# Performance work log

Hardware: AMD Instinct MI355X
Metric: run time of the kernel (lower is better)

The kernel has to match this reference:

```python
import jax, jax.numpy as jnp
import numpy as np

B, T, D, H, BUCKETS = 4, 4096, 1024, 8, 64
DH = D // H          # 128
BSZ = T // BUCKETS   # 64
TEMP = 0.75
SINK_ITERS = 5
LOG_EPS = 1e-6
GUMBEL_EPS = 1e-4


def setup_inputs() -> dict:
    key = jax.random.key(0)
    ks = jax.random.split(key, 6)
    x = jax.random.normal(ks[0], (B, T, D), dtype=jnp.float32)
    w_qkv = jax.random.normal(ks[1], (3 * D, D), dtype=jnp.float32) * 0.02   # torch Linear weight (out,in), no bias
    sort_w = jax.random.normal(ks[2], (1, H, DH, BUCKETS), dtype=jnp.float32)
    w_out = jax.random.normal(ks[3], (D, D), dtype=jnp.float32) * 0.02
    b_out = jnp.zeros((D,), dtype=jnp.float32)
    noise_u = jax.random.uniform(ks[4], (B * H, BUCKETS, BUCKETS), dtype=jnp.float32)
    return {"x": x, "w_qkv": w_qkv, "sort_w": sort_w, "w_out": w_out, "b_out": b_out, "noise_u": noise_u}


def reference(x, w_qkv, sort_w, w_out, b_out, noise_u):
    b, t, d = x.shape
    # qkv projection + merge heads -> (b*h, t, d_h)
    qkv = x @ w_qkv.T
    q, k, v = jnp.split(qkv, 3, axis=2)
    mh = lambda u: u.reshape(b, t, H, DH).transpose(0, 2, 1, 3).reshape(b * H, t, DH)
    q, k, v = mh(q), mh(k), mh(v)
    # bucket -> (b*h, buckets, bsz, d_h)
    bk = lambda u: u.reshape(b * H, BUCKETS, BSZ, DH)
    b_q, b_k, b_v = bk(q), bk(k), bk(v)
    # bucket summaries and sinkhorn sorting matrix R: (b*h, buckets, buckets)
    b_k_r = b_k.sum(axis=2)
    e_w = jnp.broadcast_to(sort_w, (b, H, DH, BUCKETS)).reshape(b * H, DH, BUCKETS)
    R = jnp.log(jax.nn.relu(jnp.einsum('bud,bdv->buv', b_k_r, e_w)) + LOG_EPS)
    gumbel = -jnp.log(-jnp.log(noise_u + GUMBEL_EPS) + GUMBEL_EPS)
    R = (R + gumbel) / TEMP
    for _ in range(SINK_ITERS):
        R = R - jax.nn.logsumexp(R, axis=2, keepdims=True)
        R = R - jax.nn.logsumexp(R, axis=1, keepdims=True)
    R = jnp.tril(jnp.exp(R), k=-1)
    # soft-permute buckets of k and v
    k_re = jnp.einsum('buv,bvtd->butd', R, b_k)
    v_re = jnp.einsum('buv,bvtd->butd', R, b_v)
    b_k2 = jnp.concatenate((k_re, b_k), axis=2)  # (bh, buckets, 2*bsz, dh)
    b_v2 = jnp.concatenate((v_re, b_v), axis=2)
    # bucketed attention (note: scale uses full model dim d, as in source)
    dots = jnp.einsum('buie,buje->buij', b_q, b_k2) * (d ** -0.5)
    attn = jax.nn.softmax(dots, axis=-1)
    out = jnp.einsum('buij,buje->buie', attn, b_v2)
    # unbucket + split heads -> (b, t, d)
    out = out.reshape(b, H, t, DH).transpose(0, 2, 1, 3).reshape(b, t, d)
    return out @ w_out.T + b_out
```

## Files before the change

### kernel.cpp

```cpp
#include <hip/hip_runtime.h>
#include <hip/hip_bf16.h>
#include <cstdint>
#include <cstddef>
#include <math.h>
#include <type_traits>

typedef __bf16 bf16;
typedef __bf16 bf16x4 __attribute__((ext_vector_type(4)));
typedef __bf16 bf16x8 __attribute__((ext_vector_type(8)));
typedef float  f32x4  __attribute__((ext_vector_type(4)));
typedef unsigned u32x2 __attribute__((ext_vector_type(2)));


__device__ inline bool input_is_fp32(const void* x) {
  const unsigned short* u = (const unsigned short*)x;
  const int lane = threadIdx.x & 63;
  const int e = (u[lane] >> 7) & 0xFF;
  return __ballot(e >= 137) != 0ULL;
}

__device__ inline float ldx(const void* p, size_t i, bool f32) {
  return f32 ? ((const float*)p)[i] : (float)((const bf16*)p)[i];
}

template<typename T>
__device__ inline bf16x8 ld8bf(const void* p, size_t i) {
  if constexpr (std::is_same<T, float>::value) {
    const f32x4* q = (const f32x4*)((const float*)p + i);
    const f32x4 a = q[0], b = q[1];
    bf16x8 r;
    r[0]=(bf16)a[0]; r[1]=(bf16)a[1]; r[2]=(bf16)a[2]; r[3]=(bf16)a[3];
    r[4]=(bf16)b[0]; r[5]=(bf16)b[1]; r[6]=(bf16)b[2]; r[7]=(bf16)b[3];
    return r;
  } else {
    return *(const bf16x8*)((const bf16*)p + i);
  }
}

__device__ __forceinline__ void gload16(const void* g, void* l) {
  __builtin_amdgcn_global_load_lds(
      (__attribute__((address_space(1))) void*)g,
      (__attribute__((address_space(3))) void*)l, 16, 0, 0);
}

__global__ __launch_bounds__(256)
void convert_to_bf16(const void* __restrict__ src, bf16* __restrict__ dst,
                     const void* __restrict__ xdet) {
  const bool f32 = input_is_fp32(xdet);
  const size_t i = ((size_t)blockIdx.x * 256 + threadIdx.x) * 8;
  if (f32) *(bf16x8*)&dst[i] = ld8bf<float>(src, i);
  else     *(bf16x8*)&dst[i] = ld8bf<bf16 >(src, i);
}

template<int EPI>
__global__ __launch_bounds__(256)
void gemm_bt(const bf16* __restrict__ A, const bf16* __restrict__ Bm,
             const void* __restrict__ bias,
             void* __restrict__ C0, bf16* __restrict__ C1, bf16* __restrict__ C2,
             const void* __restrict__ xdet, int M, int N, int K)
{
  __shared__ __align__(16) bf16 As[128*32];
  __shared__ __align__(16) bf16 Bs[128*32];
  const int tid  = threadIdx.x;
  const int wave = tid >> 6, lane = tid & 63;
  const int m0 = blockIdx.y * 128, n0 = blockIdx.x * 128;
  const int wm = (wave >> 1) * 64, wn = (wave & 1) * 64;
  const int fr = lane & 15;
  const int fk = (lane >> 4) * 8;

  const int srow = wave * 16 + (lane >> 2);
  const int scol = (lane & 3) * 8;
  const bf16* gA = A  + (size_t)(m0 + srow) * K + scol;
  const bf16* gB = Bm + (size_t)(n0 + srow) * K + scol;
  bf16* lA = &As[wave * 16 * 32];
  bf16* lB = &Bs[wave * 16 * 32];

  f32x4 acc[4][4];
  #pragma unroll
  for (int a = 0; a < 4; ++a)
    #pragma unroll
    for (int b = 0; b < 4; ++b) { f32x4 z = {0.f, 0.f, 0.f, 0.f}; acc[a][b] = z; }

  for (int k0 = 0; k0 < K; k0 += 32) {
    __syncthreads();
    gload16(gA + k0,                  lA);
    gload16(gA + (size_t)64*K + k0,   lA + 64*32);
    gload16(gB + k0,                  lB);
    gload16(gB + (size_t)64*K + k0,   lB + 64*32);
    __syncthreads();
    bf16x8 af[4], bfr[4];
    #pragma unroll
    for (int t = 0; t < 4; ++t) {
      af[t]  = *(const bf16x8*)&As[(wm + t*16 + fr)*32 + fk];
      bfr[t] = *(const bf16x8*)&Bs[(wn + t*16 + fr)*32 + fk];
    }
    #pragma unroll
    for (int tm = 0; tm < 4; ++tm)
      #pragma unroll
      for (int tn = 0; tn < 4; ++tn)
        acc[tm][tn] = __builtin_amdgcn_mfma_f32_16x16x32_bf16(af[tm], bfr[tn], acc[tm][tn], 0, 0, 0);
  }

  const int cn = lane & 15, cr = (lane >> 4) * 4;
  if constexpr (EPI == 0) {
    const int sel = n0 >> 10;
    const int cb  = (n0 & 1023) + wn;
    #pragma unroll
    for (int tm = 0; tm < 4; ++tm) {
      const int m = m0 + wm + tm*16 + cr;
      const int b = m >> 12, t = m & 4095;
      const int u = t >> 6,  i = t & 63;
      #pragma unroll
      for (int tn = 0; tn < 4; ++tn) {
        const int c = cb + tn*16 + cn;
        const int h = c >> 7, e = c & 127;
        const size_t bhu = (size_t)((b*8 + h)*64 + u);
        if (sel == 2) {
          bf16x4 w;
          #pragma unroll
          for (int r = 0; r < 4; ++r) w[r] = (bf16)acc[tm][tn][r];
          *(bf16x4*)&C2[(bhu*128 + e)*64 + i] = w;
        } else {
          bf16* dst = (sel == 0) ? (bf16*)C0 : C1;
          #pragma unroll
          for (int r = 0; r < 4; ++r)
            dst[(bhu*64 + i + r)*128 + e] = (bf16)acc[tm][tn][r];
        }
      }
    }
  } else {
    const bool f32o = input_is_fp32(xdet);
    #pragma unroll
    for (int tm = 0; tm < 4; ++tm) {
      #pragma unroll
      for (int tn = 0; tn < 4; ++tn) {
        #pragma unroll
        for (int r = 0; r < 4; ++r) {
          const int m = m0 + wm + tm*16 + cr + r;
          const int n = n0 + wn + tn*16 + cn;
          const float val = acc[tm][tn][r] + ldx(bias, n, f32o);
          if (f32o) ((float*)C0)[(size_t)m*N + n] = val;
          else      ((bf16*)C0)[(size_t)m*N + n] = (bf16)val;
        }
      }
    }
  }
}

__global__ __launch_bounds__(128)
void bksum(const bf16* __restrict__ k_ws, float* __restrict__ bkr_g)
{
  const int ug = blockIdx.x, bh = blockIdx.y, t = threadIdx.x;
  const int ul = t >> 4, e0 = (t & 15) * 8;
  const int u = ug * 8 + ul;
  const bf16* p = k_ws + ((size_t)bh*64 + u)*8192 + e0;
  float acc[8];
  #pragma unroll
  for (int j = 0; j < 8; ++j) acc[j] = 0.f;
  for (int i = 0; i < 64; ++i) {
    bf16x8 kv = *(const bf16x8*)&p[i*128];
    #pragma unroll
    for (int j = 0; j < 8; ++j) acc[j] += (float)kv[j];
  }
  float* dst = bkr_g + (size_t)bh*8192 + u*128 + e0;
  #pragma unroll
  for (int j = 0; j < 8; ++j) dst[j] = acc[j];
}

__global__ __launch_bounds__(256)
void sinkhorn_R(const float* __restrict__ bkr_g, const void* __restrict__ sort_w,
                const void* __restrict__ noise, float* __restrict__ R_buf,
                const void* __restrict__ xdet)
{
  const bool f32 = input_is_fp32(xdet);
  const int bh = blockIdx.x, h = bh & 7, tid = threadIdx.x;
  __shared__ float bkr[64*128];
  __shared__ float ew[128*64];
  __shared__ float R[64*65];

  for (int f = tid; f < 64*128; f += 256) bkr[f] = bkr_g[(size_t)bh*8192 + f];
  for (int f = tid; f < 128*64; f += 256) ew[f] = ldx(sort_w, (size_t)h*8192 + f, f32);
  __syncthreads();

  for (int f = tid; f < 64*64; f += 256) {
    const int u = f >> 6, v = f & 63;
    float s = 0.f;
    for (int e = 0; e < 128; ++e) s += bkr[u*128 + e] * ew[e*64 + v];
    s = fmaxf(s, 0.f);
    const float r  = logf(s + 1e-6f);
    const double nz = (double)ldx(noise, ((size_t)bh*64 + u)*64 + v, f32);
    const double t1 = log(nz + 1e-4);
    const double t2 = fmax(-t1 + 1e-4, 1e-30);
    const float g = (float)(-log(t2));
    R[u*65 + v] = (r + g) * (1.f / 0.75f);
  }
  __syncthreads();

  for (int it = 0; it < 5; ++it) {
    if (tid < 64) {
      float mx = -1e30f;
      for (int v = 0; v < 64; ++v) mx = fmaxf(mx, R[tid*65 + v]);
      float s = 0.f;
      for (int v = 0; v < 64; ++v) s += expf(R[tid*65 + v] - mx);
      const float l = mx + logf(s);
      for (int v = 0; v < 64; ++v) R[tid*65 + v] -= l;
    }
    __syncthreads();
    if (tid < 64) {
      float mx = -1e30f;
      for (int u = 0; u < 64; ++u) mx = fmaxf(mx, R[u*65 + tid]);
      float s = 0.f;
      for (int u = 0; u < 64; ++u) s += expf(R[u*65 + tid] - mx);
      const float l = mx + logf(s);
      for (int u = 0; u < 64; ++u) R[u*65 + tid] -= l;
    }
    __syncthreads();
  }

  for (int f = tid; f < 64*64; f += 256) {
    const int u = f >> 6, v = f & 63;
    R_buf[(size_t)bh*4096 + f] = (u > v) ? expf(R[u*65 + v]) : 0.f;
  }
}

__global__ __launch_bounds__(256)
void permute_kv(const float* __restrict__ R_buf,
                const bf16* __restrict__ Xk, const bf16* __restrict__ Xv,
                bf16* __restrict__ Ok, bf16* __restrict__ Ov, int bh0)
{
  const int tid = threadIdx.x;
  const int bhl = blockIdx.y, bh = bh0 + bhl;
  const int f0  = blockIdx.x * 256;
  const bf16* X = blockIdx.z ? Xv : Xk;
  bf16*       O = blockIdx.z ? Ov : Ok;

  __shared__ __align__(16) bf16 A_lds[64*136];
  __shared__ __align__(16) bf16 X_lds[16*1048];

  {
    const bf16* Xg = X + (size_t)bh*524288 + f0;
    const int vb = tid >> 5, c = tid & 31;
    const int dst = (c >> 1)*1048 + (c & 1)*8;
    #pragma unroll
    for (int p = 0; p < 8; ++p) {
      const int v = vb + p*8;
      *(bf16x8*)&X_lds[dst + v*16] = *(const bf16x8*)&Xg[(size_t)v*8192 + c*8];
    }
  }
  {
    const float* Rg = R_buf + (size_t)bh*4096;
    #pragma unroll
    for (int p = 0; p < 16; ++p) {
      const int idx = tid + p*256;
      const int uu = idx >> 6, vv = idx & 63;
      const float r = Rg[idx];
      const bf16 hi = (bf16)r;
      const float lo = r - (float)hi;
      A_lds[uu*136 + vv]      = hi;
      A_lds[uu*136 + 64 + vv] = (bf16)lo;
    }
  }
  __syncthreads();

  const int lane = tid & 63, wave = tid >> 6;
  const int fr = lane & 15, quad = lane >> 4;

  bf16x8 af[4][4];
  #pragma unroll
  for (int mt = 0; mt < 4; ++mt)
    #pragma unroll
    for (int ks = 0; ks < 4; ++ks)
      af[mt][ks] = *(const bf16x8*)&A_lds[(mt*16 + fr)*136 + ks*32 + quad*8];

  f32x4 acc[4][4];
  #pragma unroll
  for (int a = 0; a < 4; ++a)
    #pragma unroll
    for (int b = 0; b < 4; ++b) { f32x4 z = {0.f,0.f,0.f,0.f}; acc[a][b] = z; }

  #pragma unroll
  for (int nt = 0; nt < 4; ++nt) {
    const int g = wave*4 + nt;
    const unsigned addr = (unsigned)(size_t)
        (__attribute__((address_space(3))) bf16*)&X_lds[g*1048 + quad*128 + fr*4];
    u32x2 p0, p1, p2, p3;
    asm volatile(
      "ds_read_b64_tr_b16 %0, %4\n"
      "ds_read_b64_tr_b16 %1, %4 offset:128\n"
      "ds_read_b64_tr_b16 %2, %4 offset:1024\n"
      "ds_read_b64_tr_b16 %3, %4 offset:1152\n"
      : "=&v"(p0), "=&v"(p1), "=&v"(p2), "=&v"(p3)
      : "v"(addr));
    asm volatile("s_waitcnt lgkmcnt(0)" ::: "memory");
    __builtin_amdgcn_sched_barrier(0);
    union { u32x2 u[2]; bf16x8 v; } c0, c1;
    c0.u[0] = p0; c0.u[1] = p1;
    c1.u[0] = p2; c1.u[1] = p3;
    const bf16x8 b0 = c0.v, b1 = c1.v;
    #pragma unroll
    for (int mt = 0; mt < 4; ++mt) {
      acc[mt][nt] = __builtin_amdgcn_mfma_f32_16x16x32_bf16(af[mt][0], b0, acc[mt][nt], 0, 0, 0);
      acc[mt][nt] = __builtin_amdgcn_mfma_f32_16x16x32_bf16(af[mt][1], b1, acc[mt][nt], 0, 0, 0);
      acc[mt][nt] = __builtin_amdgcn_mfma_f32_16x16x32_bf16(af[mt][2], b0, acc[mt][nt], 0, 0, 0);
      acc[mt][nt] = __builtin_amdgcn_mfma_f32_16x16x32_bf16(af[mt][3], b1, acc[mt][nt], 0, 0, 0);
    }
  }

  bf16* Og = O + (size_t)bhl*524288 + f0;
  #pragma unroll
  for (int mt = 0; mt < 4; ++mt)
    #pragma unroll
    for (int nt = 0; nt < 4; ++nt)
      #pragma unroll
      for (int r = 0; r < 4; ++r)
        Og[(size_t)(mt*16 + quad*4 + r)*8192 + wave*64 + nt*16 + fr] = (bf16)acc[mt][nt][r];
}

__global__ __launch_bounds__(256)
void attn_mfma(const bf16* __restrict__ q_ws, const bf16* __restrict__ k_ws,
               const bf16* __restrict__ vT_ws,
               const bf16* __restrict__ kre_g, const bf16* __restrict__ vre_g,
               bf16* __restrict__ aout, int bh0)
{
  const int u = blockIdx.x, bhl = blockIdx.y, bh = bh0 + bhl;
  const int tid = threadIdx.x;
  const int lane = tid & 63, wave = tid >> 6;
  const int fr = lane & 15, quad = lane >> 4;

  __shared__ __align__(16) unsigned char smem[34048];
  float* sc = (float*)smem;
  bf16*  pA = (bf16*)smem;

  const size_t tileq = ((size_t)bh *64 + u) * 8192;
  const size_t tilel = ((size_t)bhl*64 + u) * 8192;

  {
    f32x4 dacc[4][2];
    #pragma unroll
    for (int mt = 0; mt < 4; ++mt)
      #pragma unroll
      for (int nt = 0; nt < 2; ++nt) { f32x4 z = {0.f,0.f,0.f,0.f}; dacc[mt][nt] = z; }
    #pragma unroll
    for (int ks = 0; ks < 4; ++ks) {
      bf16x8 afr[4];
      #pragma unroll
      for (int mt = 0; mt < 4; ++mt)
        afr[mt] = *(const bf16x8*)&q_ws[tileq + (size_t)(mt*16 + fr)*128 + ks*32 + quad*8];
      #pragma unroll
      for (int nt = 0; nt < 2; ++nt) {
        const int j = wave*32 + nt*16 + fr;
        bf16x8 bfr;
        if (wave < 2) bfr = *(const bf16x8*)&kre_g[tilel + (size_t)j*128 + ks*32 + quad*8];
        else          bfr = *(const bf16x8*)&k_ws[tileq + (size_t)(j - 64)*128 + ks*32 + quad*8];
        #pragma unroll
        for (int mt = 0; mt < 4; ++mt)
          dacc[mt][nt] = __builtin_amdgcn_mfma_f32_16x16x32_bf16(afr[mt], bfr, dacc[mt][nt], 0, 0, 0);
      }
    }
    #pragma unroll
    for (int mt = 0; mt < 4; ++mt)
      #pragma unroll
      for (int nt = 0; nt < 2; ++nt)
        #pragma unroll
        for (int r = 0; r < 4; ++r)
          sc[(mt*16 + quad*4 + r)*132 + wave*32 + nt*16 + fr] = dacc[mt][nt][r] * 0.03125f;
  }
  __syncthreads();

  {
    const int i = tid >> 2, jc = tid & 3;
    float pv[32];
    float mx = -1e30f;
    #pragma unroll
    for (int t = 0; t < 32; ++t) { pv[t] = sc[i*132 + jc + t*4]; mx = fmaxf(mx, pv[t]); }
    mx = fmaxf(mx, __shfl_xor(mx, 1));
    mx = fmaxf(mx, __shfl_xor(mx, 2));
    float s = 0.f;
    #pragma unroll
    for (int t = 0; t < 32; ++t) { pv[t] = expf(pv[t] - mx); s += pv[t]; }
    s += __shfl_xor(s, 1);
    s += __shfl_xor(s, 2);
    const float inv = 1.f / s;
    __syncthreads();
    #pragma unroll
    for (int t = 0; t < 32; ++t) pA[i*136 + jc + t*4] = (bf16)(pv[t] * inv);
  }
  __syncthreads();

  {
    f32x4 oacc[4][2];
    #pragma unroll
    for (int mt = 0; mt < 4; ++mt)
      #pragma unroll
      for (int nt = 0; nt < 2; ++nt) { f32x4 z = {0.f,0.f,0.f,0.f}; oacc[mt][nt] = z; }
    #pragma unroll
    for (int ks = 0; ks < 4; ++ks) {
      bf16x8 afr[4];
      #pragma unroll
      for (int mt = 0; mt < 4; ++mt)
        afr[mt] = *(const bf16x8*)&pA[(mt*16 + fr)*136 + ks*32 + quad*8];
      #pragma unroll
      for (int nt = 0; nt < 2; ++nt) {
        const int e = wave*32 + nt*16 + fr;
        bf16x8 bfr;
        if (ks < 2) bfr = *(const bf16x8*)&vre_g[tilel + (size_t)e*64 + ks*32 + quad*8];
        else        bfr = *(const bf16x8*)&vT_ws[tileq + (size_t)e*64 + (ks - 2)*32 + quad*8];
        #pragma unroll
        for (int mt = 0; mt < 4; ++mt)
          oacc[mt][nt] = __builtin_amdgcn_mfma_f32_16x16x32_bf16(afr[mt], bfr, oacc[mt][nt], 0, 0, 0);
      }
    }
    __syncthreads();
    #pragma unroll
    for (int mt = 0; mt < 4; ++mt)
      #pragma unroll
      for (int nt = 0; nt < 2; ++nt)
        #pragma unroll
        for (int r = 0; r < 4; ++r)
          pA[(mt*16 + quad*4 + r)*136 + wave*32 + nt*16 + fr] = (bf16)oacc[mt][nt][r];
  }
  __syncthreads();

  {
    const int b = bh >> 3, h = bh & 7;
    #pragma unroll
    for (int r = 0; r < 4; ++r) {
      const int f = r*2048 + tid*8;
      const int i = f >> 7, e0 = f & 127;
      bf16x8 w = *(const bf16x8*)&pA[i*136 + e0];
      *(bf16x8*)&aout[((size_t)(b*4096 + u*64 + i))*1024 + h*128 + e0] = w;
    }
  }
}

extern "C" void kernel_launch(void* const* d_in, const int* in_sizes, int n_in,
                              void* d_out, int out_size, void* d_ws, size_t ws_size,
                              hipStream_t stream)
{
  (void)in_sizes; (void)n_in; (void)out_size; (void)ws_size;
  const void* x      = d_in[0];
  const void* w_qkv  = d_in[1];
  const void* sort_w = d_in[2];
  const void* w_out  = d_in[3];
  const void* b_out  = d_in[4];
  const void* noise  = d_in[5];

  char* ws = (char*)d_ws;
  const size_t TEN = (size_t)32*64*64*128;
  const size_t HEN = TEN / 2;
  bf16* q_ws  = (bf16*)ws;
  bf16* k_ws  = q_ws + TEN;
  bf16* vT_ws = k_ws + TEN;
  bf16* xa_ws = vT_ws + TEN;

  float* bkr_g = (float*)((char*)xa_ws + (size_t)30*1024*1024);
  float* R_buf = (float*)((char*)xa_ws + (size_t)31*1024*1024);
  bf16* wqkv_bf = (bf16*)((char*)d_out + (1536<<10));
  bf16* kre = (bf16*)d_out;
  bf16* vre = kre + HEN;
  bf16* wout_bf = k_ws;

  convert_to_bf16<<<8192, 256, 0, stream>>>(x, xa_ws, x);
  convert_to_bf16<<<1536, 256, 0, stream>>>(w_qkv, wqkv_bf, x);

  gemm_bt<0><<<dim3(24,128), 256, 0, stream>>>(xa_ws, wqkv_bf, nullptr,
                                               q_ws, k_ws, vT_ws, x, 16384, 3072, 1024);

  bksum<<<dim3(8,32), 128, 0, stream>>>(k_ws, bkr_g);
  sinkhorn_R<<<32, 256, 0, stream>>>(bkr_g, sort_w, noise, R_buf, x);

  permute_kv<<<dim3(32,16,2), 256, 0, stream>>>(R_buf, k_ws, vT_ws, kre, vre, 0);
  attn_mfma<<<dim3(64,16), 256, 0, stream>>>(q_ws, k_ws, vT_ws, kre, vre, xa_ws, 0);
  permute_kv<<<dim3(32,16,2), 256, 0, stream>>>(R_buf, k_ws, vT_ws, kre, vre, 16);
  attn_mfma<<<dim3(64,16), 256, 0, stream>>>(q_ws, k_ws, vT_ws, kre, vre, xa_ws, 16);

  convert_to_bf16<<<512, 256, 0, stream>>>(w_out, wout_bf, x);
  gemm_bt<1><<<dim3(8,128), 256, 0, stream>>>(xa_ws, wout_bf, b_out,
                                              d_out, nullptr, nullptr, x, 16384, 1024, 1024);
}
```

Before: 479.2 us.

## Replace GEMM with 256x256 tile double-buffered pipelined kernel with swizzled LDS

```diff
diff --git a/kernel.cpp b/kernel.cpp
--- a/kernel.cpp
+++ b/kernel.cpp
@@ -53,92 +53,166 @@
 }
 
 template<int EPI>
-__global__ __launch_bounds__(256)
-void gemm_bt(const bf16* __restrict__ A, const bf16* __restrict__ Bm,
+__global__ __launch_bounds__(512, 2)
+void gemm256(const bf16* __restrict__ A, const bf16* __restrict__ Bm,
              const void* __restrict__ bias,
              void* __restrict__ C0, bf16* __restrict__ C1, bf16* __restrict__ C2,
              const void* __restrict__ xdet, int M, int N, int K)
 {
-  __shared__ __align__(16) bf16 As[128*32];
-  __shared__ __align__(16) bf16 Bs[128*32];
-  const int tid  = threadIdx.x;
-  const int wave = tid >> 6, lane = tid & 63;
-  const int m0 = blockIdx.y * 128, n0 = blockIdx.x * 128;
-  const int wm = (wave >> 1) * 64, wn = (wave & 1) * 64;
-  const int fr = lane & 15;
-  const int fk = (lane >> 4) * 8;
-
-  const int srow = wave * 16 + (lane >> 2);
-  const int scol = (lane & 3) * 8;
-  const bf16* gA = A  + (size_t)(m0 + srow) * K + scol;
-  const bf16* gB = Bm + (size_t)(n0 + srow) * K + scol;
-  bf16* lA = &As[wave * 16 * 32];
-  bf16* lB = &Bs[wave * 16 * 32];
-
-  f32x4 acc[4][4];
-  #pragma unroll
-  for (int a = 0; a < 4; ++a)
-    #pragma unroll
-    for (int b = 0; b < 4; ++b) { f32x4 z = {0.f, 0.f, 0.f, 0.f}; acc[a][b] = z; }
-
-  for (int k0 = 0; k0 < K; k0 += 32) {
-    __syncthreads();
-    gload16(gA + k0,                  lA);
-    gload16(gA + (size_t)64*K + k0,   lA + 64*32);
-    gload16(gB + k0,                  lB);
-    gload16(gB + (size_t)64*K + k0,   lB + 64*32);
-    __syncthreads();
-    bf16x8 af[4], bfr[4];
-    #pragma unroll
-    for (int t = 0; t < 4; ++t) {
-      af[t]  = *(const bf16x8*)&As[(wm + t*16 + fr)*32 + fk];
-      bfr[t] = *(const bf16x8*)&Bs[(wn + t*16 + fr)*32 + fk];
-    }
-    #pragma unroll
-    for (int tm = 0; tm < 4; ++tm)
-      #pragma unroll
-      for (int tn = 0; tn < 4; ++tn)
-        acc[tm][tn] = __builtin_amdgcn_mfma_f32_16x16x32_bf16(af[tm], bfr[tn], acc[tm][tn], 0, 0, 0);
-  }
-
-  const int cn = lane & 15, cr = (lane >> 4) * 4;
+  __shared__ __align__(16) bf16 lds[2][2][2][8192];
+  const int tid = threadIdx.x, wave = tid >> 6, lane = tid & 63;
+  const int fr = lane & 15, quad = lane >> 4;
+  const int m0 = blockIdx.y * 256, n0 = blockIdx.x * 256;
+  const int wm = wave >> 2, wn = wave & 3;
+  const int gsz  = (quad ^ ((fr >> 1) & 3)) * 16;
+  const int srow = wave * 32 + (lane >> 2);
+  const int sg   = ((lane & 3) ^ ((lane >> 3) & 3)) * 8;
+  const int NT = K >> 6;
+  char* ldsb = (char*)&lds[0][0][0][0];
+
+  auto stageA = [&](int buf, int kh, int t) {
+    const bf16* s = A + (size_t)(m0 + srow) * K + t*64 + kh*32 + sg;
+    char* d = ldsb + buf*65536 + kh*16384 + wave*2048;
+    gload16(s, d);
+    gload16(s + (size_t)16 * K, d + 1024);
+  };
+  auto stageB = [&](int buf, int kh, int t) {
+    const bf16* s = Bm + (size_t)(n0 + srow) * K + t*64 + kh*32 + sg;
+    char* d = ldsb + buf*65536 + 32768 + kh*16384 + wave*2048;
+    gload16(s, d);
+    gload16(s + (size_t)16 * K, d + 1024);
+  };
+  auto lda = [&](int c, int kh, int fi) {
+    return *(const bf16x8*)(ldsb + c*65536 + kh*16384 + (wm*128 + fi*16 + fr)*64 + gsz);
+  };
+  auto ldb = [&](int c, int kh, int fi) {
+    return *(const bf16x8*)(ldsb + c*65536 + 32768 + kh*16384 + (wn*64 + fi*16 + fr)*64 + gsz);
+  };
+
+  f32x4 acc[8][4];
+  #pragma unroll
+  for (int a = 0; a < 8; ++a)
+    #pragma unroll
+    for (int b = 0; b < 4; ++b) { f32x4 z = {0.f,0.f,0.f,0.f}; acc[a][b] = z; }
+
+  stageA(0, 0, 0); stageB(0, 0, 0);
+  stageA(0, 1, 0); stageB(0, 1, 0);
+  stageA(1, 0, 1); stageB(1, 0, 1);
+  asm volatile("s_waitcnt vmcnt(8)" ::: "memory");
+  __builtin_amdgcn_s_barrier();
+
+  #pragma unroll 1
+  for (int t = 0; t < NT; ++t) {
+    const int c = t & 1;
+    const bool d12 = (t + 1 < NT), d34 = (t + 2 < NT);
+    bf16x8 bfr[4], afr[4];
+
+    #pragma unroll
+    for (int n = 0; n < 4; ++n) bfr[n] = ldb(c, 0, n);
+    #pragma unroll
+    for (int m = 0; m < 4; ++m) afr[m] = lda(c, 0, m);
+    if (d12) stageA(c ^ 1, 1, t + 1);
+    __builtin_amdgcn_s_barrier();
+    asm volatile("s_waitcnt lgkmcnt(0)" ::: "memory");
+    __builtin_amdgcn_sched_barrier(0);
+    __builtin_amdgcn_s_setprio(1);
+    #pragma unroll
+    for (int m = 0; m < 4; ++m)
+      #pragma unroll
+      for (int n = 0; n < 4; ++n)
+        acc[m][n] = __builtin_amdgcn_mfma_f32_16x16x32_bf16(afr[m], bfr[n], acc[m][n], 0, 0, 0);
+    __builtin_amdgcn_s_setprio(0);
+    __builtin_amdgcn_s_barrier();
+
+    #pragma unroll
+    for (int m = 0; m < 4; ++m) afr[m] = lda(c, 0, 4 + m);
+    if (d12) stageB(c ^ 1, 1, t + 1);
+    __builtin_amdgcn_s_barrier();
+    asm volatile("s_waitcnt lgkmcnt(0)" ::: "memory");
+    __builtin_amdgcn_sched_barrier(0);
+    __builtin_amdgcn_s_setprio(1);
+    #pragma unroll
+    for (int m = 0; m < 4; ++m)
+      #pragma unroll
+      for (int n = 0; n < 4; ++n)
+        acc[4 + m][n] = __builtin_amdgcn_mfma_f32_16x16x32_bf16(afr[m], bfr[n], acc[4 + m][n], 0, 0, 0);
+    __builtin_amdgcn_s_setprio(0);
+    if (t < NT - 1) { asm volatile("s_waitcnt vmcnt(8)" ::: "memory"); }
+    else            { asm volatile("s_waitcnt vmcnt(0)" ::: "memory"); }
+    __builtin_amdgcn_s_barrier();
+
+    #pragma unroll
+    for (int n = 0; n < 4; ++n) bfr[n] = ldb(c, 1, n);
+    #pragma unroll
+    for (int m = 0; m < 4; ++m) afr[m] = lda(c, 1, m);
+    if (d34) stageA(c, 0, t + 2);
+    __builtin_amdgcn_s_barrier();
+    asm volatile("s_waitcnt lgkmcnt(0)" ::: "memory");
+    __builtin_amdgcn_sched_barrier(0);
+    __builtin_amdgcn_s_setprio(1);
+    #pragma unroll
+    for (int m = 0; m < 4; ++m)
+      #pragma unroll
+      for (int n = 0; n < 4; ++n)
+        acc[m][n] = __builtin_amdgcn_mfma_f32_16x16x32_bf16(afr[m], bfr[n], acc[m][n], 0, 0, 0);
+    __builtin_amdgcn_s_setprio(0);
+    __builtin_amdgcn_s_barrier();
+
+    #pragma unroll
+    for (int m = 0; m < 4; ++m) afr[m] = lda(c, 1, 4 + m);
+    if (d34) stageB(c, 0, t + 2);
+    __builtin_amdgcn_s_barrier();
+    asm volatile("s_waitcnt lgkmcnt(0)" ::: "memory");
+    __builtin_amdgcn_sched_barrier(0);
+    __builtin_amdgcn_s_setprio(1);
+    #pragma unroll
+    for (int m = 0; m < 4; ++m)
+      #pragma unroll
+      for (int n = 0; n < 4; ++n)
+        acc[4 + m][n] = __builtin_amdgcn_mfma_f32_16x16x32_bf16(afr[m], bfr[n], acc[4 + m][n], 0, 0, 0);
+    __builtin_amdgcn_s_setprio(0);
+    if (t < NT - 2)       { asm volatile("s_waitcnt vmcnt(8)" ::: "memory"); }
+    else if (t == NT - 2) { asm volatile("s_waitcnt vmcnt(4)" ::: "memory"); }
+    __builtin_amdgcn_s_barrier();
+  }
+
   if constexpr (EPI == 0) {
     const int sel = n0 >> 10;
-    const int cb  = (n0 & 1023) + wn;
-    #pragma unroll
-    for (int tm = 0; tm < 4; ++tm) {
-      const int m = m0 + wm + tm*16 + cr;
-      const int b = m >> 12, t = m & 4095;
-      const int u = t >> 6,  i = t & 63;
-      #pragma unroll
-      for (int tn = 0; tn < 4; ++tn) {
-        const int c = cb + tn*16 + cn;
-        const int h = c >> 7, e = c & 127;
+    const int cb  = (n0 & 1023) + wn * 64;
+    #pragma unroll
+    for (int im = 0; im < 8; ++im) {
+      const int mrow = m0 + wm*128 + im*16 + quad*4;
+      const int b = mrow >> 12, tt = mrow & 4095;
+      const int u = tt >> 6, i = tt & 63;
+      #pragma unroll
+      for (int nn = 0; nn < 4; ++nn) {
+        const int cc = cb + nn*16 + fr;
+        const int h = cc >> 7, e = cc & 127;
         const size_t bhu = (size_t)((b*8 + h)*64 + u);
         if (sel == 2) {
           bf16x4 w;
           #pragma unroll
-          for (int r = 0; r < 4; ++r) w[r] = (bf16)acc[tm][tn][r];
+          for (int r = 0; r < 4; ++r) w[r] = (bf16)acc[im][nn][r];
           *(bf16x4*)&C2[(bhu*128 + e)*64 + i] = w;
         } else {
           bf16* dst = (sel == 0) ? (bf16*)C0 : C1;
           #pragma unroll
           for (int r = 0; r < 4; ++r)
-            dst[(bhu*64 + i + r)*128 + e] = (bf16)acc[tm][tn][r];
+            dst[(bhu*64 + i + r)*128 + e] = (bf16)acc[im][nn][r];
         }
       }
     }
   } else {
     const bool f32o = input_is_fp32(xdet);
     #pragma unroll
-    for (int tm = 0; tm < 4; ++tm) {
-      #pragma unroll
-      for (int tn = 0; tn < 4; ++tn) {
+    for (int im = 0; im < 8; ++im) {
+      #pragma unroll
+      for (int nn = 0; nn < 4; ++nn) {
         #pragma unroll
         for (int r = 0; r < 4; ++r) {
-          const int m = m0 + wm + tm*16 + cr + r;
-          const int n = n0 + wn + tn*16 + cn;
-          const float val = acc[tm][tn][r] + ldx(bias, n, f32o);
+          const int m = m0 + wm*128 + im*16 + quad*4 + r;
+          const int n = n0 + wn*64 + nn*16 + fr;
+          const float val = acc[im][nn][r] + ldx(bias, n, f32o);
           if (f32o) ((float*)C0)[(size_t)m*N + n] = val;
           else      ((bf16*)C0)[(size_t)m*N + n] = (bf16)val;
         }
@@ -463,8 +537,8 @@
   convert_to_bf16<<<8192, 256, 0, stream>>>(x, xa_ws, x);
   convert_to_bf16<<<1536, 256, 0, stream>>>(w_qkv, wqkv_bf, x);
 
-  gemm_bt<0><<<dim3(24,128), 256, 0, stream>>>(xa_ws, wqkv_bf, nullptr,
-                                               q_ws, k_ws, vT_ws, x, 16384, 3072, 1024);
+  gemm256<0><<<dim3(12,64), 512, 0, stream>>>(xa_ws, wqkv_bf, nullptr,
+                                              q_ws, k_ws, vT_ws, x, 16384, 3072, 1024);
 
   bksum<<<dim3(8,32), 128, 0, stream>>>(k_ws, bkr_g);
   sinkhorn_R<<<32, 256, 0, stream>>>(bkr_g, sort_w, noise, R_buf, x);
@@ -475,6 +549,6 @@
   attn_mfma<<<dim3(64,16), 256, 0, stream>>>(q_ws, k_ws, vT_ws, kre, vre, xa_ws, 16);
 
   convert_to_bf16<<<512, 256, 0, stream>>>(w_out, wout_bf, x);
-  gemm_bt<1><<<dim3(8,128), 256, 0, stream>>>(xa_ws, wout_bf, b_out,
-                                              d_out, nullptr, nullptr, x, 16384, 1024, 1024);
-}
+  gemm256<1><<<dim3(4,64), 512, 0, stream>>>(xa_ws, wout_bf, b_out,
+                                             d_out, nullptr, nullptr, x, 16384, 1024, 1024);
+}
```

Measured after the change: 434.3 us. 1.1x faster.
